# Performance work log

Hardware: AMD Instinct MI355X
Metric: run time of the kernel (lower is better)

Reference implementation:

```python
import jax, jax.numpy as jnp
import numpy as np

L, H, A, I, V, B, T = 6, 1024, 1024, 4096, 50277, 4, 2048
EPS = 1e-5
NEG = -1e38  # numerically equivalent to -inf init for the WKV exponent


def setup_inputs() -> dict:
    key = jax.random.key(0)
    ks = iter(jax.random.split(key, 32))
    def nrm(shape, s):
        return jax.random.normal(next(ks), shape, jnp.float32) * s
    def uni(shape):
        return jax.random.uniform(next(ks), shape, jnp.float32)
    inp = {
        'input_ids': jax.random.randint(next(ks), (B, T), 0, V),
        'embed': nrm((V, H), 0.02),
        'pre_ln_w': jnp.ones((H,), jnp.float32), 'pre_ln_b': jnp.zeros((H,), jnp.float32),
        'post_ln_w': jnp.ones((H,), jnp.float32), 'post_ln_b': jnp.zeros((H,), jnp.float32),
        'ln1_w': jnp.ones((L, H), jnp.float32), 'ln1_b': jnp.zeros((L, H), jnp.float32),
        'ln2_w': jnp.ones((L, H), jnp.float32), 'ln2_b': jnp.zeros((L, H), jnp.float32),
        'att_mix_k': uni((L, 1, 1, H)), 'att_mix_v': uni((L, 1, 1, H)), 'att_mix_r': uni((L, 1, 1, H)),
        'att_wk': nrm((L, A, H), H ** -0.5), 'att_wv': nrm((L, A, H), H ** -0.5),
        'att_wr': nrm((L, A, H), H ** -0.5), 'att_wo': nrm((L, H, A), A ** -0.5),
        'time_decay': nrm((L, A), 0.5), 'time_first': nrm((L, A), 0.5),
        'ffn_mix_k': uni((L, 1, 1, H)), 'ffn_mix_r': uni((L, 1, 1, H)),
        'ffn_wk': nrm((L, I, H), H ** -0.5), 'ffn_wr': nrm((L, H, H), H ** -0.5),
        'ffn_wv': nrm((L, H, I), I ** -0.5),
    }
    return inp


def layer_norm(x, w, b):
    mu = jnp.mean(x, axis=-1, keepdims=True)
    var = jnp.var(x, axis=-1, keepdims=True)
    return (x - mu) * jax.lax.rsqrt(var + EPS) * w + b


def time_shift(x):  # previous token, zero at t=0
    return jnp.pad(x, ((0, 0), (1, 0), (0, 0)))[:, :-1]


def wkv_scan(u, w, k, v):
    """RWKV WKV recurrence with max-exponent stabilization.
    u,w: [A]; k,v: [B,T,A] -> [B,T,A]."""
    def step(carry, kv):
        a, b, p = carry           # [B,A] each
        kt, vt = kv               # [B,A]
        q = jnp.maximum(p, u + kt)
        wt = jnp.exp(u + kt - q)
        sc = jnp.exp(p - q)
        out = (a * sc + wt * vt) / (b * sc + wt)
        q2 = jnp.maximum(p + w, kt)
        s1 = jnp.exp(p + w - q2)
        s2 = jnp.exp(kt - q2)
        return (s1 * a + s2 * vt, s1 * b + s2, q2), out
    bsz = k.shape[0]
    init = (jnp.zeros((bsz, A), k.dtype), jnp.zeros((bsz, A), k.dtype),
            jnp.full((bsz, A), NEG, k.dtype))
    _, out = jax.lax.scan(step, init, (k.transpose(1, 0, 2), v.transpose(1, 0, 2)))
    return out.transpose(1, 0, 2)


def reference(input_ids, embed, pre_ln_w, pre_ln_b, post_ln_w, post_ln_b,
              ln1_w, ln1_b, ln2_w, ln2_b,
              att_mix_k, att_mix_v, att_mix_r, att_wk, att_wv, att_wr, att_wo,
              time_decay, time_first, ffn_mix_k, ffn_mix_r, ffn_wk, ffn_wr, ffn_wv):
    h = layer_norm(embed[input_ids], pre_ln_w, pre_ln_b)
    for i in range(L):
        # --- attention (time mixing) ---
        x = layer_norm(h, ln1_w[i], ln1_b[i])
        prev = time_shift(x)
        k = (att_mix_k[i] * x + (1 - att_mix_k[i]) * prev) @ att_wk[i].T
        v = (att_mix_v[i] * x + (1 - att_mix_v[i]) * prev) @ att_wv[i].T
        r = jax.nn.sigmoid((att_mix_r[i] * x + (1 - att_mix_r[i]) * prev) @ att_wr[i].T)
        y = wkv_scan(time_first[i], -jnp.exp(time_decay[i]), k, v)
        h = h + (r * y) @ att_wo[i].T
        # --- feed forward (channel mixing) ---
        x = layer_norm(h, ln2_w[i], ln2_b[i])
        prev = time_shift(x)
        kk = jnp.square(jax.nn.relu((ffn_mix_k[i] * x + (1 - ffn_mix_k[i]) * prev) @ ffn_wk[i].T))
        rr = jax.nn.sigmoid((ffn_mix_r[i] * x + (1 - ffn_mix_r[i]) * prev) @ ffn_wr[i].T)
        h = h + rr * (kk @ ffn_wv[i].T)
    return layer_norm(h, post_ln_w, post_ln_b)
```

## Files before the change

### kernel.cpp

```cpp
#include <hip/hip_runtime.h>
#include <stdint.h>


#define LNUM 6
#define HD   1024
#define AD   1024
#define TT   2048
#define NTOK 8192
#define EPSF 1e-5f
#define NEGF (-1e38f)

#define WKV_C  32
#define WKV_NC 64
#define NCH    4096

typedef __attribute__((ext_vector_type(8))) short bf16x8;
typedef __attribute__((ext_vector_type(4))) float f32x4;

__device__ __forceinline__ unsigned short f2bf(float f) {
  union { float f; uint32_t u; } c; c.f = f;
  uint32_t r = c.u + 0x7fffu + ((c.u >> 16) & 1u);
  return (unsigned short)(r >> 16);
}

__device__ __forceinline__ void gld_lds16(const void* g, const void* l) {
  __builtin_amdgcn_global_load_lds(
      (const __attribute__((address_space(1))) void*)(uintptr_t)g,
      (__attribute__((address_space(3))) void*)(uint32_t)(uintptr_t)l,
      16, 0, 0);
}

enum { EP_NONE = 0, EP_SIG = 1, EP_RELUSQ = 2, EP_ADD = 3, EP_MULADD = 4 };

template <int EPI>
__global__ __launch_bounds__(256) void gemm_nt(
    const unsigned short* __restrict__ Aact,
    const unsigned short* __restrict__ Bw,
    float* __restrict__ Co,
    unsigned short* __restrict__ Cb,
    const float* __restrict__ aux,
    int K, int M)
{
  __shared__ unsigned short sA[4][128 * 32];
  __shared__ unsigned short sB[4][128 * 32];
  const int tid  = threadIdx.x;
  const int lane = tid & 63;
  const int wave = tid >> 6;
  const int quad = lane >> 4;
  const int r16  = lane & 15;
  const int wm = wave >> 1, wn = wave & 1;
  const int m0 = blockIdx.x * 128;
  const int n0 = blockIdx.y * 128;

  f32x4 acc[4][4];
#pragma unroll
  for (int i = 0; i < 4; ++i)
#pragma unroll
    for (int j = 0; j < 4; ++j) acc[i][j] = (f32x4){0.f, 0.f, 0.f, 0.f};

  const int wbase = wave * 64;
  const int nk = K >> 5;

  const int row0 = tid >> 2,          kc0 = tid & 3;
  const int row1 = (256 + tid) >> 2,  kc1 = (256 + tid) & 3;

  auto STAGE = [&](int buf, int kt) {
    const int k0 = kt << 5;
    gld_lds16(Aact + (size_t)(m0 + row0) * K + k0 + kc0 * 8,
              (const char*)sA[buf] + wbase * 16);
    gld_lds16(Bw   + (size_t)(n0 + row0) * K + k0 + kc0 * 8,
              (const char*)sB[buf] + wbase * 16);
    gld_lds16(Aact + (size_t)(m0 + row1) * K + k0 + kc1 * 8,
              (const char*)sA[buf] + (256 + wbase) * 16);
    gld_lds16(Bw   + (size_t)(n0 + row1) * K + k0 + kc1 * 8,
              (const char*)sB[buf] + (256 + wbase) * 16);
  };

  STAGE(0, 0);
  if (nk > 1) STAGE(1, 1);

  for (int kt = 0; kt < nk; ++kt) {
    if (kt + 2 < nk) {
      STAGE((kt + 2) & 3, kt + 2);
      asm volatile("s_waitcnt vmcnt(8)" ::: "memory");
    } else if (kt + 1 < nk) {
      asm volatile("s_waitcnt vmcnt(4)" ::: "memory");
    } else {
      asm volatile("s_waitcnt vmcnt(0)" ::: "memory");
    }
    __builtin_amdgcn_s_barrier();
    asm volatile("" ::: "memory");

    const unsigned short* a_s = sA[kt & 3];
    const unsigned short* b_s = sB[kt & 3];
    bf16x8 af[4], bfr[4];
#pragma unroll
    for (int i = 0; i < 4; ++i) {
      af[i]  = *(const bf16x8*)(a_s + (wm * 64 + i * 16 + r16) * 32 + quad * 8);
      bfr[i] = *(const bf16x8*)(b_s + (wn * 64 + i * 16 + r16) * 32 + quad * 8);
    }
#pragma unroll
    for (int i = 0; i < 4; ++i)
#pragma unroll
      for (int j = 0; j < 4; ++j)
        acc[i][j] = __builtin_amdgcn_mfma_f32_16x16x32_bf16(af[i], bfr[j], acc[i][j], 0, 0, 0);
  }

#pragma unroll
  for (int i = 0; i < 4; ++i) {
    const int ar = m0 + wm * 64 + i * 16 + quad * 4;
#pragma unroll
    for (int j = 0; j < 4; ++j) {
      const int cc = n0 + wn * 64 + j * 16 + r16;
#pragma unroll
      for (int r = 0; r < 4; ++r) {
        const size_t idx = (size_t)(ar + r) * M + cc;
        const float v = acc[i][j][r];
        if constexpr (EPI == EP_NONE)   Co[idx] = v;
        if constexpr (EPI == EP_SIG)    Co[idx] = 1.f / (1.f + __expf(-v));
        if constexpr (EPI == EP_RELUSQ) { const float t = fmaxf(v, 0.f); Cb[idx] = f2bf(t * t); }
        if constexpr (EPI == EP_ADD)    Co[idx] += v;
        if constexpr (EPI == EP_MULADD) Co[idx] += aux[idx] * v;
      }
    }
  }
}

__global__ __launch_bounds__(256) void ln_kernel(
    const float* __restrict__ in, const int* __restrict__ ids,
    const float* __restrict__ emb,
    const float* __restrict__ gw, const float* __restrict__ gb,
    float* __restrict__ out)
{
  const int n = blockIdx.x, tid = threadIdx.x;
  const float* src = ids ? (emb + (size_t)ids[n] * HD) : (in + (size_t)n * HD);
  const float4 v = ((const float4*)src)[tid];
  float s  = v.x + v.y + v.z + v.w;
  float s2 = v.x * v.x + v.y * v.y + v.z * v.z + v.w * v.w;
#pragma unroll
  for (int off = 32; off > 0; off >>= 1) {
    s  += __shfl_down(s, off);
    s2 += __shfl_down(s2, off);
  }
  __shared__ float red[8];
  const int wv = tid >> 6, ln = tid & 63;
  if (ln == 0) { red[wv] = s; red[4 + wv] = s2; }
  __syncthreads();
  if (tid == 0) {
    const float S  = red[0] + red[1] + red[2] + red[3];
    const float S2 = red[4] + red[5] + red[6] + red[7];
    const float mu = S * (1.f / HD);
    const float var = S2 * (1.f / HD) - mu * mu;
    red[0] = mu; red[1] = rsqrtf(var + EPSF);
  }
  __syncthreads();
  const float mu = red[0], rs = red[1];
  const float4 w4 = ((const float4*)gw)[tid];
  const float4 b4 = ((const float4*)gb)[tid];
  float4 o;
  o.x = (v.x - mu) * rs * w4.x + b4.x;
  o.y = (v.y - mu) * rs * w4.y + b4.y;
  o.z = (v.z - mu) * rs * w4.z + b4.z;
  o.w = (v.w - mu) * rs * w4.w + b4.w;
  ((float4*)(out + (size_t)n * HD))[tid] = o;
}

__global__ __launch_bounds__(256) void lnmix_kernel(
    const float* __restrict__ h,
    const float* __restrict__ gw, const float* __restrict__ gb,
    const float* __restrict__ m0p, const float* __restrict__ m1p, const float* __restrict__ m2p,
    ushort4* __restrict__ o0, ushort4* __restrict__ o1, ushort4* __restrict__ o2)
{
  const int n = blockIdx.x, tid = threadIdx.x;
  const int t = n & (TT - 1);
  const float4 vc = ((const float4*)(h + (size_t)n * HD))[tid];
  float4 vp = make_float4(0.f, 0.f, 0.f, 0.f);
  if (t != 0) vp = ((const float4*)(h + (size_t)(n - 1) * HD))[tid];

  float sc  = vc.x + vc.y + vc.z + vc.w;
  float sc2 = vc.x * vc.x + vc.y * vc.y + vc.z * vc.z + vc.w * vc.w;
  float sp  = vp.x + vp.y + vp.z + vp.w;
  float sp2 = vp.x * vp.x + vp.y * vp.y + vp.z * vp.z + vp.w * vp.w;
#pragma unroll
  for (int off = 32; off > 0; off >>= 1) {
    sc  += __shfl_down(sc, off);
    sc2 += __shfl_down(sc2, off);
    sp  += __shfl_down(sp, off);
    sp2 += __shfl_down(sp2, off);
  }
  __shared__ float red[16];
  const int wv = tid >> 6, ln = tid & 63;
  if (ln == 0) { red[wv] = sc; red[4 + wv] = sc2; red[8 + wv] = sp; red[12 + wv] = sp2; }
  __syncthreads();
  if (tid == 0) {
    float S  = red[0] + red[1] + red[2] + red[3];
    float S2 = red[4] + red[5] + red[6] + red[7];
    float mu = S * (1.f / HD);
    float var = S2 * (1.f / HD) - mu * mu;
    red[0] = mu; red[1] = rsqrtf(var + EPSF);
    S  = red[8] + red[9] + red[10] + red[11];
    S2 = red[12] + red[13] + red[14] + red[15];
    mu = S * (1.f / HD);
    var = S2 * (1.f / HD) - mu * mu;
    red[2] = mu; red[3] = rsqrtf(var + EPSF);
  }
  __syncthreads();
  const float muc = red[0], rsc = red[1];
  const float mup = red[2], rsp = red[3];
  const float4 w4 = ((const float4*)gw)[tid];
  const float4 b4 = ((const float4*)gb)[tid];
  float4 xc, xp;
  xc.x = (vc.x - muc) * rsc * w4.x + b4.x;
  xc.y = (vc.y - muc) * rsc * w4.y + b4.y;
  xc.z = (vc.z - muc) * rsc * w4.z + b4.z;
  xc.w = (vc.w - muc) * rsc * w4.w + b4.w;
  if (t != 0) {
    xp.x = (vp.x - mup) * rsp * w4.x + b4.x;
    xp.y = (vp.y - mup) * rsp * w4.y + b4.y;
    xp.z = (vp.z - mup) * rsp * w4.z + b4.z;
    xp.w = (vp.w - mup) * rsp * w4.w + b4.w;
  } else {
    xp = make_float4(0.f, 0.f, 0.f, 0.f);
  }

  const size_t o = (size_t)n * 256 + tid;
  float4 m = ((const float4*)m0p)[tid];
  ushort4 r;
  r.x = f2bf(m.x * xc.x + (1.f - m.x) * xp.x);
  r.y = f2bf(m.y * xc.y + (1.f - m.y) * xp.y);
  r.z = f2bf(m.z * xc.z + (1.f - m.z) * xp.z);
  r.w = f2bf(m.w * xc.w + (1.f - m.w) * xp.w);
  o0[o] = r;
  m = ((const float4*)m1p)[tid];
  r.x = f2bf(m.x * xc.x + (1.f - m.x) * xp.x);
  r.y = f2bf(m.y * xc.y + (1.f - m.y) * xp.y);
  r.z = f2bf(m.z * xc.z + (1.f - m.z) * xp.z);
  r.w = f2bf(m.w * xc.w + (1.f - m.w) * xp.w);
  o1[o] = r;
  if (o2) {
    m = ((const float4*)m2p)[tid];
    r.x = f2bf(m.x * xc.x + (1.f - m.x) * xp.x);
    r.y = f2bf(m.y * xc.y + (1.f - m.y) * xp.y);
    r.z = f2bf(m.z * xc.z + (1.f - m.z) * xp.z);
    r.w = f2bf(m.w * xc.w + (1.f - m.w) * xp.w);
    o2[o] = r;
  }
}

__global__ __launch_bounds__(256) void wkv_p1(
    const float* __restrict__ kx, const float* __restrict__ vx,
    const float* __restrict__ tdecay,
    float* __restrict__ la, float* __restrict__ lb, float* __restrict__ lp)
{
  const int c = blockIdx.x * 256 + threadIdx.x;
  const int a = c & (AD - 1);
  const int b = c >> 10;
  const int j = blockIdx.y;
  const float w = -__expf(tdecay[a]);
  const size_t base = ((size_t)b * TT + (size_t)j * WKV_C) * AD + a;
  float A = 0.f, Bb = 0.f, p = NEGF;
#pragma unroll 4
  for (int t = 0; t < WKV_C; ++t) {
    const float kt = kx[base + (size_t)t * AD];
    const float vt = vx[base + (size_t)t * AD];
    const float pn = fmaxf(p + w, kt);
    const float s1 = __expf(p + w - pn);
    const float s2 = __expf(kt - pn);
    A = s1 * A + s2 * vt;
    Bb = s1 * Bb + s2;
    p = pn;
  }
  const int o = j * NCH + c;
  la[o] = A; lb[o] = Bb; lp[o] = p;
}

__global__ __launch_bounds__(256) void wkv_p2(
    const float* __restrict__ la, const float* __restrict__ lb,
    const float* __restrict__ lp, const float* __restrict__ tdecay,
    float* __restrict__ sa, float* __restrict__ sb, float* __restrict__ sp)
{
  const int c = blockIdx.x * 256 + threadIdx.x;
  const int a = c & (AD - 1);
  const float wC = -__expf(tdecay[a]) * (float)WKV_C;
  float A = 0.f, Bb = 0.f, p = NEGF;
  for (int j = 0; j < WKV_NC; ++j) {
    const int o = j * NCH + c;
    sa[o] = A; sb[o] = Bb; sp[o] = p;
    const float A2 = la[o], B2 = lb[o], p2 = lp[o];
    const float pn = fmaxf(p + wC, p2);
    const float e1 = __expf(p + wC - pn);
    const float e2 = __expf(p2 - pn);
    A = e1 * A + e2 * A2;
    Bb = e1 * Bb + e2 * B2;
    p = pn;
  }
}

__global__ __launch_bounds__(256) void wkv_p3(
    const float* __restrict__ kx, const float* __restrict__ vx,
    const float* __restrict__ rx,
    const float* __restrict__ tfirst, const float* __restrict__ tdecay,
    const float* __restrict__ sa, const float* __restrict__ sb,
    const float* __restrict__ sp,
    unsigned short* __restrict__ ry)
{
  const int c = blockIdx.x * 256 + threadIdx.x;
  const int a = c & (AD - 1);
  const int b = c >> 10;
  const int j = blockIdx.y;
  const float u = tfirst[a];
  const float w = -__expf(tdecay[a]);
  const size_t base = ((size_t)b * TT + (size_t)j * WKV_C) * AD + a;
  const int o = j * NCH + c;
  float A = sa[o], Bb = sb[o], p = sp[o];
#pragma unroll 2
  for (int t = 0; t < WKV_C; ++t) {
    const size_t off = base + (size_t)t * AD;
    const float kt = kx[off], vt = vx[off];
    const float q  = fmaxf(p, u + kt);
    const float wt = __expf(u + kt - q);
    const float sc = __expf(p - q);
    const float y  = (A * sc + wt * vt) / (Bb * sc + wt);
    ry[off] = f2bf(y * rx[off]);
    const float pn = fmaxf(p + w, kt);
    const float s1 = __expf(p + w - pn);
    const float s2 = __expf(kt - pn);
    A = s1 * A + s2 * vt;
    Bb = s1 * Bb + s2;
    p = pn;
  }
}

__global__ __launch_bounds__(256) void f2b_kernel(const float* __restrict__ in,
                                                  unsigned short* __restrict__ out, int n4)
{
  const int i = blockIdx.x * 256 + threadIdx.x;
  if (i >= n4) return;
  const float4 v = ((const float4*)in)[i];
  ushort4 r;
  r.x = f2bf(v.x); r.y = f2bf(v.y); r.z = f2bf(v.z); r.w = f2bf(v.w);
  ((ushort4*)out)[i] = r;
}

extern "C" void kernel_launch(void* const* d_in, const int* in_sizes, int n_in,
                              void* d_out, int out_size, void* d_ws, size_t ws_size,
                              hipStream_t stream)
{
  (void)in_sizes; (void)n_in; (void)out_size; (void)ws_size;
  const int*   ids   = (const int*)d_in[0];
  const float* emb   = (const float*)d_in[1];
  const float* prew  = (const float*)d_in[2];
  const float* preb  = (const float*)d_in[3];
  const float* postw = (const float*)d_in[4];
  const float* postb = (const float*)d_in[5];
  const float* ln1w  = (const float*)d_in[6];
  const float* ln1b  = (const float*)d_in[7];
  const float* ln2w  = (const float*)d_in[8];
  const float* ln2b  = (const float*)d_in[9];
  const float* amk   = (const float*)d_in[10];
  const float* amv   = (const float*)d_in[11];
  const float* amr   = (const float*)d_in[12];
  const float* awk   = (const float*)d_in[13];
  const float* awv   = (const float*)d_in[14];
  const float* awr   = (const float*)d_in[15];
  const float* awo   = (const float*)d_in[16];
  const float* td    = (const float*)d_in[17];
  const float* tf    = (const float*)d_in[18];
  const float* fmk   = (const float*)d_in[19];
  const float* fmr   = (const float*)d_in[20];
  const float* fwk   = (const float*)d_in[21];
  const float* fwr   = (const float*)d_in[22];
  const float* fwv   = (const float*)d_in[23];

  char* ws = (char*)d_ws;
  float* h  = (float*)(ws + 0);
  float* x  = (float*)(ws + 33554432);
  float* kb = (float*)(ws + 67108864);
  float* vb = (float*)(ws + 100663296);
  float* rb = (float*)(ws + 134217728);
  unsigned short* ab = (unsigned short*)(ws + 167772160);
  unsigned short* wb = (unsigned short*)(ws + 234881024);

  unsigned short* xk = ab;
  unsigned short* xv = ab + 8388608;
  unsigned short* xr = ab + 16777216;
  unsigned short* ry = ab + 25165824;

  float* wla = x;
  float* wlb = x + WKV_NC * NCH;
  float* wlp = x + 2 * WKV_NC * NCH;
  float* wsa = x + 3 * WKV_NC * NCH;
  float* wsb = x + 4 * WKV_NC * NCH;
  float* wsp = x + 5 * WKV_NC * NCH;

  const dim3 blk(256);
  const dim3 g1(NTOK / 128, 1024 / 128);
  const dim3 g2(NTOK / 128, 4096 / 128);
  const dim3 gw(NCH / 256, WKV_NC);

  ln_kernel<<<NTOK, blk, 0, stream>>>(nullptr, ids, emb, prew, preb, h);

  for (int i = 0; i < LNUM; ++i) {
    f2b_kernel<<<1024, blk, 0, stream>>>(awk + (size_t)i * 1048576, wb + 0,       262144);
    f2b_kernel<<<1024, blk, 0, stream>>>(awv + (size_t)i * 1048576, wb + 1048576, 262144);
    f2b_kernel<<<1024, blk, 0, stream>>>(awr + (size_t)i * 1048576, wb + 2097152, 262144);
    f2b_kernel<<<1024, blk, 0, stream>>>(awo + (size_t)i * 1048576, wb + 3145728, 262144);
    f2b_kernel<<<4096, blk, 0, stream>>>(fwk + (size_t)i * 4194304, wb + 4194304, 1048576);
    f2b_kernel<<<1024, blk, 0, stream>>>(fwr + (size_t)i * 1048576, wb + 8388608, 262144);
    f2b_kernel<<<4096, blk, 0, stream>>>(fwv + (size_t)i * 4194304, wb + 9437184, 1048576);

    lnmix_kernel<<<NTOK, blk, 0, stream>>>(h, ln1w + i * HD, ln1b + i * HD,
                                           amk + i * HD, amv + i * HD, amr + i * HD,
                                           (ushort4*)xk, (ushort4*)xv, (ushort4*)xr);
    gemm_nt<EP_NONE><<<g1, blk, 0, stream>>>(xk, wb + 0,       kb, nullptr, nullptr, 1024, 1024);
    gemm_nt<EP_NONE><<<g1, blk, 0, stream>>>(xv, wb + 1048576, vb, nullptr, nullptr, 1024, 1024);
    gemm_nt<EP_SIG ><<<g1, blk, 0, stream>>>(xr, wb + 2097152, rb, nullptr, nullptr, 1024, 1024);
    wkv_p1<<<gw, blk, 0, stream>>>(kb, vb, td + i * AD, wla, wlb, wlp);
    wkv_p2<<<NCH / 256, blk, 0, stream>>>(wla, wlb, wlp, td + i * AD, wsa, wsb, wsp);
    wkv_p3<<<gw, blk, 0, stream>>>(kb, vb, rb, tf + i * AD, td + i * AD, wsa, wsb, wsp, ry);
    gemm_nt<EP_ADD ><<<g1, blk, 0, stream>>>(ry, wb + 3145728, h, nullptr, nullptr, 1024, 1024);

    lnmix_kernel<<<NTOK, blk, 0, stream>>>(h, ln2w + i * HD, ln2b + i * HD,
                                           fmk + i * HD, fmr + i * HD, nullptr,
                                           (ushort4*)kb, (ushort4*)vb, nullptr);
    gemm_nt<EP_RELUSQ><<<g2, blk, 0, stream>>>((unsigned short*)kb, wb + 4194304, nullptr, ab, nullptr, 1024, 4096);
    gemm_nt<EP_SIG   ><<<g1, blk, 0, stream>>>((unsigned short*)vb, wb + 8388608, rb, nullptr, nullptr, 1024, 1024);
    gemm_nt<EP_MULADD><<<g1, blk, 0, stream>>>(ab, wb + 9437184, h, nullptr, rb, 4096, 1024);
  }

  ln_kernel<<<NTOK, blk, 0, stream>>>(h, nullptr, nullptr, postw, postb, (float*)d_out);
}
```

Measured before the change: 2.904 ms.

## Swizzle GEMM LDS layout, batch K/V/R GEMMs via grid z, merge weight casts

Applies an XOR swizzle to the k-chunk position of staged A/B tiles in LDS and reads fragments with the matching swizzle, aiming to remove LDS bank conflicts in the MFMA fragment loads. The three attention projection GEMMs are merged into one launch using blockIdx.z, which relies on xk/xv/xr, the bf16 weights and kb/vb/rb being laid out at fixed strides. The seven per-layer weight-conversion launches are folded into one kernel. Together these cut launch overhead and fill the GPU better, at the cost of hardcoded buffer offsets and a per-element branch in the epilogue.

```diff
diff --git a/kernel.cpp b/kernel.cpp
--- a/kernel.cpp
+++ b/kernel.cpp
@@ -30,7 +30,7 @@
       16, 0, 0);
 }
 
-enum { EP_NONE = 0, EP_SIG = 1, EP_RELUSQ = 2, EP_ADD = 3, EP_MULADD = 4 };
+enum { EP_NONE = 0, EP_SIG = 1, EP_RELUSQ = 2, EP_ADD = 3, EP_MULADD = 4, EP_KVR = 5 };
 
 template <int EPI>
 __global__ __launch_bounds__(256) void gemm_nt(
@@ -52,6 +52,13 @@
   const int m0 = blockIdx.x * 128;
   const int n0 = blockIdx.y * 128;
 
+  if constexpr (EPI == EP_KVR) {
+    const int z = blockIdx.z;
+    Aact += (size_t)z * 8388608;
+    Bw   += (size_t)z * 1048576;
+    Co   += (size_t)z * 8388608;
+  }
+
   f32x4 acc[4][4];
 #pragma unroll
   for (int i = 0; i < 4; ++i)
@@ -61,23 +68,29 @@
   const int wbase = wave * 64;
   const int nk = K >> 5;
 
-  const int row0 = tid >> 2,          kc0 = tid & 3;
-  const int row1 = (256 + tid) >> 2,  kc1 = (256 + tid) & 3;
+  const int row0 = tid >> 2,         kc0 = tid & 3;
+  const int row1 = 64 + row0,        kc1 = kc0;
+  const int sw0 = (row0 >> 1) & 3;
+  const int kg0 = kc0 ^ sw0;
+  const int kg1 = kc1 ^ sw0;
 
   auto STAGE = [&](int buf, int kt) {
     const int k0 = kt << 5;
-    gld_lds16(Aact + (size_t)(m0 + row0) * K + k0 + kc0 * 8,
+    gld_lds16(Aact + (size_t)(m0 + row0) * K + k0 + kg0 * 8,
               (const char*)sA[buf] + wbase * 16);
-    gld_lds16(Bw   + (size_t)(n0 + row0) * K + k0 + kc0 * 8,
+    gld_lds16(Bw   + (size_t)(n0 + row0) * K + k0 + kg0 * 8,
               (const char*)sB[buf] + wbase * 16);
-    gld_lds16(Aact + (size_t)(m0 + row1) * K + k0 + kc1 * 8,
+    gld_lds16(Aact + (size_t)(m0 + row1) * K + k0 + kg1 * 8,
               (const char*)sA[buf] + (256 + wbase) * 16);
-    gld_lds16(Bw   + (size_t)(n0 + row1) * K + k0 + kc1 * 8,
+    gld_lds16(Bw   + (size_t)(n0 + row1) * K + k0 + kg1 * 8,
               (const char*)sB[buf] + (256 + wbase) * 16);
   };
 
   STAGE(0, 0);
   if (nk > 1) STAGE(1, 1);
+
+  const int swr = (r16 >> 1) & 3;
+  const int qsw = (quad ^ swr) * 8;
 
   for (int kt = 0; kt < nk; ++kt) {
     if (kt + 2 < nk) {
@@ -96,8 +109,8 @@
     bf16x8 af[4], bfr[4];
 #pragma unroll
     for (int i = 0; i < 4; ++i) {
-      af[i]  = *(const bf16x8*)(a_s + (wm * 64 + i * 16 + r16) * 32 + quad * 8);
-      bfr[i] = *(const bf16x8*)(b_s + (wn * 64 + i * 16 + r16) * 32 + quad * 8);
+      af[i]  = *(const bf16x8*)(a_s + (wm * 64 + i * 16 + r16) * 32 + qsw);
+      bfr[i] = *(const bf16x8*)(b_s + (wn * 64 + i * 16 + r16) * 32 + qsw);
     }
 #pragma unroll
     for (int i = 0; i < 4; ++i)
@@ -121,6 +134,9 @@
         if constexpr (EPI == EP_RELUSQ) { const float t = fmaxf(v, 0.f); Cb[idx] = f2bf(t * t); }
         if constexpr (EPI == EP_ADD)    Co[idx] += v;
         if constexpr (EPI == EP_MULADD) Co[idx] += aux[idx] * v;
+        if constexpr (EPI == EP_KVR) {
+          Co[idx] = (blockIdx.z == 2) ? (1.f / (1.f + __expf(-v))) : v;
+        }
       }
     }
   }
@@ -331,15 +347,25 @@
   }
 }
 
-__global__ __launch_bounds__(256) void f2b_kernel(const float* __restrict__ in,
-                                                  unsigned short* __restrict__ out, int n4)
-{
-  const int i = blockIdx.x * 256 + threadIdx.x;
-  if (i >= n4) return;
-  const float4 v = ((const float4*)in)[i];
+__global__ __launch_bounds__(256) void f2b7_kernel(
+    const float* __restrict__ s0, const float* __restrict__ s1,
+    const float* __restrict__ s2, const float* __restrict__ s3,
+    const float* __restrict__ s4, const float* __restrict__ s5,
+    const float* __restrict__ s6, ushort4* __restrict__ wb4)
+{
+  const size_t i = (size_t)blockIdx.x * 256 + threadIdx.x;
+  const float* s; size_t rel;
+  if      (i <  262144) { s = s0; rel = i; }
+  else if (i <  524288) { s = s1; rel = i -  262144; }
+  else if (i <  786432) { s = s2; rel = i -  524288; }
+  else if (i < 1048576) { s = s3; rel = i -  786432; }
+  else if (i < 2097152) { s = s4; rel = i - 1048576; }
+  else if (i < 2359296) { s = s5; rel = i - 2097152; }
+  else                  { s = s6; rel = i - 2359296; }
+  const float4 v = ((const float4*)s)[rel];
   ushort4 r;
   r.x = f2bf(v.x); r.y = f2bf(v.y); r.z = f2bf(v.z); r.w = f2bf(v.w);
-  ((ushort4*)out)[i] = r;
+  wb4[i] = r;
 }
 
 extern "C" void kernel_launch(void* const* d_in, const int* in_sizes, int n_in,
@@ -396,25 +422,22 @@
   const dim3 blk(256);
   const dim3 g1(NTOK / 128, 1024 / 128);
   const dim3 g2(NTOK / 128, 4096 / 128);
+  const dim3 gkvr(NTOK / 128, 1024 / 128, 3);
   const dim3 gw(NCH / 256, WKV_NC);
 
   ln_kernel<<<NTOK, blk, 0, stream>>>(nullptr, ids, emb, prew, preb, h);
 
   for (int i = 0; i < LNUM; ++i) {
-    f2b_kernel<<<1024, blk, 0, stream>>>(awk + (size_t)i * 1048576, wb + 0,       262144);
-    f2b_kernel<<<1024, blk, 0, stream>>>(awv + (size_t)i * 1048576, wb + 1048576, 262144);
-    f2b_kernel<<<1024, blk, 0, stream>>>(awr + (size_t)i * 1048576, wb + 2097152, 262144);
-    f2b_kernel<<<1024, blk, 0, stream>>>(awo + (size_t)i * 1048576, wb + 3145728, 262144);
-    f2b_kernel<<<4096, blk, 0, stream>>>(fwk + (size_t)i * 4194304, wb + 4194304, 1048576);
-    f2b_kernel<<<1024, blk, 0, stream>>>(fwr + (size_t)i * 1048576, wb + 8388608, 262144);
-    f2b_kernel<<<4096, blk, 0, stream>>>(fwv + (size_t)i * 4194304, wb + 9437184, 1048576);
+    f2b7_kernel<<<13312, blk, 0, stream>>>(
+        awk + (size_t)i * 1048576, awv + (size_t)i * 1048576,
+        awr + (size_t)i * 1048576, awo + (size_t)i * 1048576,
+        fwk + (size_t)i * 4194304, fwr + (size_t)i * 1048576,
+        fwv + (size_t)i * 4194304, (ushort4*)wb);
 
     lnmix_kernel<<<NTOK, blk, 0, stream>>>(h, ln1w + i * HD, ln1b + i * HD,
                                            amk + i * HD, amv + i * HD, amr + i * HD,
                                            (ushort4*)xk, (ushort4*)xv, (ushort4*)xr);
-    gemm_nt<EP_NONE><<<g1, blk, 0, stream>>>(xk, wb + 0,       kb, nullptr, nullptr, 1024, 1024);
-    gemm_nt<EP_NONE><<<g1, blk, 0, stream>>>(xv, wb + 1048576, vb, nullptr, nullptr, 1024, 1024);
-    gemm_nt<EP_SIG ><<<g1, blk, 0, stream>>>(xr, wb + 2097152, rb, nullptr, nullptr, 1024, 1024);
+    gemm_nt<EP_KVR><<<gkvr, blk, 0, stream>>>(xk, wb, kb, nullptr, nullptr, 1024, 1024);
     wkv_p1<<<gw, blk, 0, stream>>>(kb, vb, td + i * AD, wla, wlb, wlp);
     wkv_p2<<<NCH / 256, blk, 0, stream>>>(wla, wlb, wlp, td + i * AD, wsa, wsb, wsp);
     wkv_p3<<<gw, blk, 0, stream>>>(kb, vb, rb, tf + i * AD, td + i * AD, wsa, wsb, wsp, ry);
```

Measured after the change: 2.750 ms. -5.3%, faster.
